# Optimization experiments

Measured on AMD Instinct MI355X. Metric: run time of the kernel, lower is better.

Reference implementation:

```python
import jax, jax.numpy as jnp
import numpy as np

B, N, DEG = 64, 256, 16          # graphs, nodes per graph, avg degree
FIN, OUT, DEP, HID = 256, 256, 64, 256
E = B * N * DEG                   # 262144 edges (no self loops)
NN = B * N                        # 16384 total nodes


def setup_inputs() -> dict:
    key = jax.random.key(0)
    ks = jax.random.split(key, 12)
    s = 0.05
    x = jax.random.normal(ks[0], (NN, FIN), jnp.float32)
    # random edges within each graph block, guaranteed no self loops
    src = jax.random.randint(ks[1], (E,), 0, N)
    dst = (src + jax.random.randint(ks[2], (E,), 1, N)) % N
    gid = jnp.repeat(jnp.arange(B) * N, N * DEG)
    edge_index = jnp.stack([src + gid, dst + gid]).astype(jnp.int32)
    edge_attr = jax.random.normal(ks[3], (E, DEP), jnp.float32)
    WA = jax.random.normal(ks[4], (OUT, FIN), jnp.float32) * s
    WB = jax.random.normal(ks[5], (OUT, DEP), jnp.float32) * s
    gcn_bias = jnp.zeros((OUT,), jnp.float32)

    def gru_p(k, insz):
        k1, k2, k3, k4 = jax.random.split(k, 4)
        return (jax.random.normal(k1, (3 * HID, insz), jnp.float32) * s,
                jax.random.normal(k2, (3 * HID, HID), jnp.float32) * s,
                jax.random.normal(k3, (3 * HID,), jnp.float32) * s,
                jax.random.normal(k4, (3 * HID,), jnp.float32) * s)

    w_ih0, w_hh0, b_ih0, b_hh0 = gru_p(ks[6], OUT)
    w_ih1, w_hh1, b_ih1, b_hh1 = gru_p(ks[7], HID)
    w_ih2, w_hh2, b_ih2, b_hh2 = gru_p(ks[8], HID)
    lin_W = jax.random.normal(ks[9], (2, 5 * HID), jnp.float32) * s
    lin_b = jnp.zeros((2,), jnp.float32)
    return dict(x=x, edge_attr=edge_attr, edge_index=edge_index, WA=WA, WB=WB,
                gcn_bias=gcn_bias,
                w_ih0=w_ih0, w_hh0=w_hh0, b_ih0=b_ih0, b_hh0=b_hh0,
                w_ih1=w_ih1, w_hh1=w_hh1, b_ih1=b_ih1, b_hh1=b_hh1,
                w_ih2=w_ih2, w_hh2=w_hh2, b_ih2=b_ih2, b_hh2=b_hh2,
                lin_W=lin_W, lin_b=lin_b)


def _gru_layer(seq, w_ih, w_hh, b_ih, b_hh):
    # seq: [B, T, in] -> ([B, T, HID], final h [B, HID]); torch GRU gate math
    xp = jnp.einsum('bti,gi->btg', seq, w_ih) + b_ih  # precompute input projections

    def step(h, xt):
        gh = h @ w_hh.T + b_hh
        xr, xz, xn = jnp.split(xt, 3, axis=-1)
        hr, hz, hn = jnp.split(gh, 3, axis=-1)
        r = jax.nn.sigmoid(xr + hr)
        z = jax.nn.sigmoid(xz + hz)
        n = jnp.tanh(xn + r * hn)
        h = (1.0 - z) * n + z * h
        return h, h

    h0 = jnp.zeros((seq.shape[0], HID), seq.dtype)
    hT, ys = jax.lax.scan(step, h0, jnp.swapaxes(xp, 0, 1))
    return jnp.swapaxes(ys, 0, 1), hT


def _forward(x, edge_attr, WA, WB, gcn_bias,
             w_ih0, w_hh0, b_ih0, b_hh0,
             w_ih1, w_hh1, b_ih1, b_hh1,
             w_ih2, w_hh2, b_ih2, b_hh2,
             lin_W, lin_b, edge_index):
    # --- myGCNConv: add_remaining_self_loops (none exist), degree norm ---
    loop = jnp.arange(NN, dtype=edge_index.dtype)
    row = jnp.concatenate([edge_index[0], loop])
    col = jnp.concatenate([edge_index[1], loop])
    ea = jnp.concatenate([edge_attr, jnp.ones((NN, DEP), edge_attr.dtype)], axis=0)
    deg = jax.ops.segment_sum(jnp.ones(row.shape, x.dtype), col, num_segments=NN)
    dinv = jnp.where(deg > 0, deg ** -0.5, 0.0)
    norm = dinv[row] * dinv[col]
    # message: norm * tanh(A(x_j) * B(edge_attr)); project nodes once, gather
    Ax = (x @ WA.T)[row]                       # [E+NN, OUT]
    Be = ea @ WB.T                             # [E+NN, OUT]
    msg = norm[:, None] * jnp.tanh(Ax * Be)
    # aggr='mean': scatter-sum / incoming-degree (>=1 after self loops)
    agg = jax.ops.segment_sum(msg, col, num_segments=NN) / jnp.maximum(deg, 1.0)[:, None]
    node = jnp.tanh(agg + gcn_bias)            # model-level Tanh

    # --- GRU (3 layers) over per-graph node sequences (equal lengths) ---
    seq = node.reshape(B, N, OUT)
    hts = []
    for p in ((w_ih0, w_hh0, b_ih0, b_hh0),
              (w_ih1, w_hh1, b_ih1, b_hh1),
              (w_ih2, w_hh2, b_ih2, b_hh2)):
        seq, hT = _gru_layer(seq, *p)
        hts.append(hT)

    avg_pool = seq.sum(axis=1) / N
    max_pool = seq.max(axis=1)
    pool = jnp.concatenate(hts + [max_pool, avg_pool], axis=1)  # [B, 5*HID]
    return jax.nn.softmax(pool @ lin_W.T + lin_b, axis=1)


def reference(x, edge_attr, edge_index, WA, WB, gcn_bias,
              w_ih0, w_hh0, b_ih0, b_hh0,
              w_ih1, w_hh1, b_ih1, b_hh1,
              w_ih2, w_hh2, b_ih2, b_hh2,
              lin_W, lin_b):
    return _forward(x, edge_attr, WA, WB, gcn_bias,
                    w_ih0, w_hh0, b_ih0, b_hh0,
                    w_ih1, w_hh1, b_ih1, b_hh1,
                    w_ih2, w_hh2, b_ih2, b_hh2,
                    lin_W, lin_b, edge_index)
```

## Files before the change

kernel.cpp:

```cpp
#include <hip/hip_runtime.h>
#include <math.h>

#define NN   16384
#define NE   262144
#define NB   64
#define SEQT 256
#define DEP  64
#define DOUT 256
#define G3   768
#define GK   256
#define ECAP 32

typedef _Float16 h2_t   __attribute__((ext_vector_type(2)));
typedef _Float16 f16x4  __attribute__((ext_vector_type(4)));
typedef _Float16 f16x8  __attribute__((ext_vector_type(8)));
typedef float    f32x4  __attribute__((ext_vector_type(4)));

static __device__ __forceinline__ h2_t pk(float a, float b) {
    return (h2_t)__builtin_amdgcn_cvt_pkrtz(a, b);
}

static __device__ __forceinline__ float fast_sigmoid(float v) {
    return __builtin_amdgcn_rcpf(1.f + __expf(-v));
}
static __device__ __forceinline__ float fast_tanh(float v) {
    return 1.f - 2.f * __builtin_amdgcn_rcpf(1.f + __expf(2.f * v));
}

static __device__ __forceinline__ void bar_lds() {
    asm volatile("s_waitcnt lgkmcnt(0)\n\ts_barrier" ::: "memory");
}

__global__ void k_count(const int* __restrict__ ei, int* deg) {
    int e = blockIdx.x * 256 + threadIdx.x;
    if (e < NE) atomicAdd(&deg[ei[NE + e]], 1);
}

__global__ __launch_bounds__(1024) void k_scan_offs(const int* __restrict__ deg,
                                                    int* __restrict__ offs,
                                                    float* __restrict__ dinv) {
    __shared__ int lds[1024];
    const int tid = threadIdx.x;
    const int v0 = tid * 16;
    int loc[16];
    int s = 0;
#pragma unroll
    for (int i = 0; i < 16; ++i) {
        int d = deg[v0 + i];
        loc[i] = s;
        s += d;
        dinv[v0 + i] = rsqrtf((float)(d + 1));
    }
    lds[tid] = s;
    __syncthreads();
    for (int off = 1; off < 1024; off <<= 1) {
        int x = (tid >= off) ? lds[tid - off] : 0;
        __syncthreads();
        lds[tid] += x;
        __syncthreads();
    }
    int base = lds[tid] - s;
#pragma unroll
    for (int i = 0; i < 16; ++i) offs[v0 + i] = base + loc[i];
}

__global__ void k_fill(const int* __restrict__ ei, const int* __restrict__ offs,
                       int* cursor, int* __restrict__ eidx) {
    int e = blockIdx.x * 256 + threadIdx.x;
    if (e < NE) {
        int c = ei[NE + e];
        int pos = offs[c] + atomicAdd(&cursor[c], 1);
        eidx[pos] = e;
    }
}

__global__ void k_bself(const float* __restrict__ WB, float* Bself) {
    int f = threadIdx.x;
    float s = 0.f;
#pragma unroll
    for (int d = 0; d < DEP; ++d) s += WB[f * DEP + d];
    Bself[f] = s;
}

__global__ void k_bias_fold(const float* __restrict__ bi0, const float* __restrict__ bh0,
                            const float* __restrict__ bi1, const float* __restrict__ bh1,
                            const float* __restrict__ bi2, const float* __restrict__ bh2,
                            float* __restrict__ o) {
    int j = blockIdx.x * 256 + threadIdx.x;
    int l = j / G3, r = j % G3;
    const float* bi = (l == 0) ? bi0 : (l == 1) ? bi1 : bi2;
    const float* bh = (l == 0) ? bh0 : (l == 1) ? bh1 : bh2;
    o[j] = bi[r] + (r < 512 ? bh[r] : 0.f);
}

__global__ void k_cvt_all(const float* __restrict__ x,  const float* __restrict__ wa,
                          const float* __restrict__ w0, const float* __restrict__ w1,
                          const float* __restrict__ w2,
                          _Float16* __restrict__ xo,  _Float16* __restrict__ wao,
                          _Float16* __restrict__ w0o, _Float16* __restrict__ w1o,
                          _Float16* __restrict__ w2o) {
    size_t i = ((size_t)blockIdx.x * 256 + threadIdx.x) * 4;
    const size_t B0 = 4194304, B1 = B0 + 65536, B2 = B1 + 196608, B3 = B2 + 196608;
    const float* in; _Float16* out; size_t off;
    if      (i < B0) { in = x;  out = xo;  off = i; }
    else if (i < B1) { in = wa; out = wao; off = i - B0; }
    else if (i < B2) { in = w0; out = w0o; off = i - B1; }
    else if (i < B3) { in = w1; out = w1o; off = i - B2; }
    else             { in = w2; out = w2o; off = i - B3; }
    float4 v = *(const float4*)(in + off);
    *(h2_t*)(out + off)     = pk(v.x, v.y);
    *(h2_t*)(out + off + 2) = pk(v.z, v.w);
}

template <bool F16OUT>
__global__ __launch_bounds__(256) void k_gemm16(const _Float16* __restrict__ A16,
                                                const _Float16* __restrict__ B16,
                                                const float* __restrict__ bias,
                                                void* __restrict__ Cout,
                                                int M, int N) {
    const int tid  = threadIdx.x;
    const int lane = tid & 63;
    const int wv   = tid >> 6;
    const int m0   = blockIdx.x * 128 + wv * 32;
    const int n0   = blockIdx.y * 128;
    const int ml   = lane & 15;
    const int quad = lane >> 4;

    const _Float16* ap0 = A16 + (size_t)(m0 + ml) * GK + quad * 8;
    const _Float16* ap1 = ap0 + (size_t)16 * GK;
    const _Float16* bp0 = B16 + (size_t)(n0 + ml) * GK + quad * 8;

    f32x4 acc[2][8];
#pragma unroll
    for (int i = 0; i < 2; ++i)
#pragma unroll
        for (int j = 0; j < 8; ++j) acc[i][j] = (f32x4){0.f, 0.f, 0.f, 0.f};

#pragma unroll 2
    for (int k0 = 0; k0 < GK; k0 += 32) {
        f16x8 a0 = *(const f16x8*)(ap0 + k0);
        f16x8 a1 = *(const f16x8*)(ap1 + k0);
#pragma unroll
        for (int nf = 0; nf < 8; ++nf) {
            f16x8 bf = *(const f16x8*)(bp0 + (size_t)nf * 16 * GK + k0);
            acc[0][nf] = __builtin_amdgcn_mfma_f32_16x16x32_f16(a0, bf, acc[0][nf], 0, 0, 0);
            acc[1][nf] = __builtin_amdgcn_mfma_f32_16x16x32_f16(a1, bf, acc[1][nf], 0, 0, 0);
        }
    }

#pragma unroll
    for (int mf = 0; mf < 2; ++mf)
#pragma unroll
        for (int nf = 0; nf < 8; ++nf) {
            const int col = n0 + nf * 16 + ml;
            const float bv = bias ? bias[col] : 0.f;
#pragma unroll
            for (int r = 0; r < 4; ++r) {
                const int row = m0 + mf * 16 + quad * 4 + r;
                float v = acc[mf][nf][r] + bv;
                if (F16OUT)
                    ((_Float16*)Cout)[(size_t)row * N + col] = (_Float16)v;
                else
                    ((float*)Cout)[(size_t)row * N + col] = v;
            }
        }
}

__global__ __launch_bounds__(256) void k_gcn(const float* __restrict__ Ax,
                                             const float* __restrict__ WB,
                                             const float* __restrict__ edge_attr,
                                             const int* __restrict__ ei,
                                             const int* __restrict__ eidx,
                                             const int* __restrict__ offs,
                                             const int* __restrict__ deg,
                                             const float* __restrict__ dinv,
                                             const float* __restrict__ Bself,
                                             const float* __restrict__ gcn_bias,
                                             _Float16* __restrict__ node16) {
    const int v = blockIdx.x;
    const int f = threadIdx.x;

    float wb[64];
#pragma unroll
    for (int d4 = 0; d4 < 16; ++d4) {
        float4 t = *(const float4*)&WB[f * DEP + d4 * 4];
        wb[d4 * 4 + 0] = t.x; wb[d4 * 4 + 1] = t.y;
        wb[d4 * 4 + 2] = t.z; wb[d4 * 4 + 3] = t.w;
    }

    __shared__ float ea_s[ECAP * 64];
    __shared__ int   es_s[ECAP];
    __shared__ int   src_s[ECAP];
    __shared__ float nrm_s[ECAP];

    const int   base = offs[v];
    const int   cnt  = deg[v];
    const float dv   = dinv[v];
    float acc = 0.f;

    for (int c0 = 0; c0 < cnt; c0 += ECAP) {
        const int n = min(ECAP, cnt - c0);
        if (f < n) {
            int e = eidx[base + c0 + f];
            es_s[f] = e;
            int s = ei[e];
            src_s[f] = s;
            nrm_s[f] = dinv[s] * dv;
        }
        __syncthreads();
        for (int idx = f; idx < n * 64; idx += 256) {
            int el = idx >> 6, d = idx & 63;
            ea_s[idx] = edge_attr[(size_t)es_s[el] * DEP + d];
        }
        __syncthreads();
        for (int i = 0; i < n; ++i) {
            float ax = Ax[(size_t)src_s[i] * DOUT + f];
            float be = 0.f;
#pragma unroll
            for (int d = 0; d < 64; ++d) be = fmaf(wb[d], ea_s[i * 64 + d], be);
            acc = fmaf(nrm_s[i], fast_tanh(ax * be), acc);
        }
        __syncthreads();
    }
    acc += dv * dv * fast_tanh(Ax[(size_t)v * DOUT + f] * Bself[f]);
    float nv = fast_tanh(acc / (float)(cnt + 1) + gcn_bias[f]);
    node16[(size_t)v * DOUT + f] = (_Float16)nv;
}

__global__ __launch_bounds__(512, 2) void k_gru_scan(const _Float16* __restrict__ xp16,
                                                     const float* __restrict__ w_hh,
                                                     const float* __restrict__ b_hh,
                                                     _Float16* __restrict__ y16,
                                                     float* __restrict__ hT_all,
                                                     int layer,
                                                     const float* __restrict__ lin_W,
                                                     const float* __restrict__ lin_b,
                                                     float* __restrict__ out) {
    const int tid  = threadIdx.x;
    const int b    = blockIdx.x;
    const int lane = tid & 63;
    const int wv   = tid >> 6;
    const int m    = lane & 15;
    const int quad = lane >> 4;
    const int p    = (m >> 3) & 1;
    const int rsel = m & 3;
    const int j    = wv * 32 + p * 16 + quad * 4 + rsel;
    const bool wr  = (m & 4) == 0;

    f16x8 A[6][8];
#pragma unroll
    for (int rb = 0; rb < 6; ++rb) {
        const int lr  = rb * 16 + m;
        const int row = ((lr >> 5) << 8) + wv * 32 + (lr & 31);
#pragma unroll
        for (int kt = 0; kt < 8; ++kt) {
            const float* wp = w_hh + (size_t)row * 256 + kt * 32 + quad * 8;
            float4 a0 = *(const float4*)wp;
            float4 a1 = *(const float4*)(wp + 4);
            union { f16x8 v; h2_t h[4]; } u;
            u.h[0] = pk(a0.x, a0.y); u.h[1] = pk(a0.z, a0.w);
            u.h[2] = pk(a1.x, a1.y); u.h[3] = pk(a1.z, a1.w);
            A[rb][kt] = u.v;
        }
    }

    const float bhn = b_hh[512 + j];

    __shared__ _Float16 h16[2][256];
    __shared__ float    pool[1280];
    __shared__ float    red[512];

    float h_old = 0.f;
    if (tid < 256) h16[0][tid] = (_Float16)0.f;
    __syncthreads();

    const _Float16* xpb  = xp16 + (size_t)b * SEQT * G3;
    _Float16*       yb16 = y16  + (size_t)b * SEQT * DOUT;

    float mx = -1e30f, sm = 0.f;

    _Float16 pxr = xpb[j], pxz = xpb[256 + j], pxn = xpb[512 + j];

    for (int t = 0; t < SEQT; ++t) {
        const float xr = (float)pxr;
        const float xz = (float)pxz;
        const float xn = (float)pxn;
        {
            const _Float16* xq = xpb + (size_t)(t + 1) * G3 + j;
            pxr = xq[0]; pxz = xq[256]; pxn = xq[512];
        }

        const _Float16* hcur = h16[t & 1];
        f32x4 C[6];
#pragma unroll
        for (int rb = 0; rb < 6; ++rb) C[rb] = (f32x4){0.f, 0.f, 0.f, 0.f};

#pragma unroll
        for (int kt = 0; kt < 8; ++kt) {
            union { f16x8 v; float4 f; } Bk;
            Bk.f = *(const float4*)&hcur[kt * 32 + quad * 8];
#pragma unroll
            for (int rb = 0; rb < 6; ++rb)
                C[rb] = __builtin_amdgcn_mfma_f32_16x16x32_f16(A[rb][kt], Bk.v, C[rb], 0, 0, 0);
        }

        float gh[3];
#pragma unroll
        for (int g = 0; g < 3; ++g) {
            const float lo01 = (rsel & 1) ? C[2 * g][1] : C[2 * g][0];
            const float lo23 = (rsel & 1) ? C[2 * g][3] : C[2 * g][2];
            const float lo   = (rsel & 2) ? lo23 : lo01;
            const float hi01 = (rsel & 1) ? C[2 * g + 1][1] : C[2 * g + 1][0];
            const float hi23 = (rsel & 1) ? C[2 * g + 1][3] : C[2 * g + 1][2];
            const float hi   = (rsel & 2) ? hi23 : hi01;
            gh[g] = p ? hi : lo;
        }

        const float r  = fast_sigmoid(xr + gh[0]);
        const float z  = fast_sigmoid(xz + gh[1]);
        const float n  = fast_tanh(xn + r * (gh[2] + bhn));
        const float hn = n + z * (h_old - n);
        h_old = hn;
        if (wr) {
            h16[(t & 1) ^ 1][j] = (_Float16)hn;
            if (layer < 2) {
                yb16[(size_t)t * DOUT + j] = (_Float16)hn;
                if (t == SEQT - 1) hT_all[layer * NB * 256 + b * 256 + j] = hn;
            }
        }
        if (layer == 2) { mx = fmaxf(mx, hn); sm += hn; }

        bar_lds();
    }

    if (layer == 2) {
        if (wr) {
            pool[j]        = hT_all[b * 256 + j];
            pool[256 + j]  = hT_all[NB * 256 + b * 256 + j];
            pool[512 + j]  = h_old;
            pool[768 + j]  = mx;
            pool[1024 + j] = sm * (1.f / 256.f);
        }
        __syncthreads();
        if (tid < 256) {
            float p0 = 0.f, p1 = 0.f;
            for (int i = tid; i < 1280; i += 256) {
                float pv = pool[i];
                p0 = fmaf(lin_W[i], pv, p0);
                p1 = fmaf(lin_W[1280 + i], pv, p1);
            }
            red[tid] = p0; red[256 + tid] = p1;
        }
        __syncthreads();
        if (tid == 0) {
            float l0 = lin_b[0], l1 = lin_b[1];
            for (int i = 0; i < 256; ++i) { l0 += red[i]; l1 += red[256 + i]; }
            float m2 = fmaxf(l0, l1);
            float e0 = __expf(l0 - m2), e1 = __expf(l1 - m2);
            float s = e0 + e1;
            out[b * 2 + 0] = e0 / s;
            out[b * 2 + 1] = e1 / s;
        }
    }
}

extern "C" void kernel_launch(void* const* d_in, const int* in_sizes, int n_in,
                              void* d_out, int out_size, void* d_ws, size_t ws_size,
                              hipStream_t stream) {
    const float* x         = (const float*)d_in[0];
    const float* edge_attr = (const float*)d_in[1];
    const int*   ei        = (const int*)d_in[2];
    const float* WA        = (const float*)d_in[3];
    const float* WB        = (const float*)d_in[4];
    const float* gcn_bias  = (const float*)d_in[5];
    const float* w_ih[3] = {(const float*)d_in[6],  (const float*)d_in[10], (const float*)d_in[14]};
    const float* w_hh[3] = {(const float*)d_in[7],  (const float*)d_in[11], (const float*)d_in[15]};
    const float* b_ih[3] = {(const float*)d_in[8],  (const float*)d_in[12], (const float*)d_in[16]};
    const float* b_hh[3] = {(const float*)d_in[9],  (const float*)d_in[13], (const float*)d_in[17]};
    const float* lin_W = (const float*)d_in[18];
    const float* lin_b = (const float*)d_in[19];
    float* out = (float*)d_out;

    char* p = (char*)d_ws;
    auto alloc = [&](size_t bytes) {
        char* r = p;
        p += (bytes + 255) & ~(size_t)255;
        return r;
    };
    int*   deg    = (int*)alloc((size_t)NN * 4);
    int*   offs   = (int*)alloc((size_t)NN * 4);
    int*   cursor = (int*)alloc((size_t)NN * 4);
    float* dinv   = (float*)alloc((size_t)NN * 4);
    int*   eidx   = (int*)alloc((size_t)NE * 4);
    float* Bself  = (float*)alloc(256 * 4);
    float* hT     = (float*)alloc(2 * NB * 256 * 4);
    float* bias768 = (float*)alloc(3 * G3 * 4);
    float* Ax     = (float*)alloc((size_t)NN * DOUT * 4);
    _Float16* xp16 = (_Float16*)alloc((size_t)NN * G3 * 2);

    _Float16* node16 = (_Float16*)alloc((size_t)NN * DOUT * 2);
    _Float16* yA16   = (_Float16*)alloc((size_t)NN * DOUT * 2);
    _Float16* x16    = (_Float16*)alloc((size_t)NN * DOUT * 2);
    _Float16* yB16   = x16;
    _Float16* WA16   = (_Float16*)alloc((size_t)256 * 256 * 2);
    _Float16* wih16[3];
    for (int l = 0; l < 3; ++l) wih16[l] = (_Float16*)alloc((size_t)G3 * 256 * 2);

    hipMemsetAsync(deg, 0, (size_t)3 * NN * 4, stream);
    k_count<<<NE / 256, 256, 0, stream>>>(ei, deg);
    k_scan_offs<<<1, 1024, 0, stream>>>(deg, offs, dinv);
    k_fill<<<NE / 256, 256, 0, stream>>>(ei, offs, cursor, eidx);
    k_bself<<<1, 256, 0, stream>>>(WB, Bself);
    k_bias_fold<<<9, 256, 0, stream>>>(b_ih[0], b_hh[0], b_ih[1], b_hh[1],
                                       b_ih[2], b_hh[2], bias768);
    k_cvt_all<<<4736, 256, 0, stream>>>(x, WA, w_ih[0], w_ih[1], w_ih[2],
                                        x16, WA16, wih16[0], wih16[1], wih16[2]);

    {
        dim3 g(NN / 128, 256 / 128);
        k_gemm16<false><<<g, 256, 0, stream>>>(x16, WA16, nullptr, Ax, NN, 256);
    }
    k_gcn<<<NN, 256, 0, stream>>>(Ax, WB, edge_attr, ei, eidx, offs, deg, dinv,
                                  Bself, gcn_bias, node16);

    const _Float16* in16 = node16;
    _Float16* y16_outs[3] = {yA16, yB16, yA16};
    for (int l = 0; l < 3; ++l) {
        dim3 g(NN / 128, G3 / 128);
        k_gemm16<true><<<g, 256, 0, stream>>>(in16, wih16[l], bias768 + l * G3,
                                              xp16, NN, G3);
        k_gru_scan<<<NB, 512, 0, stream>>>(xp16, w_hh[l], b_hh[l], y16_outs[l],
                                           hT, l, lin_W, lin_b, out);
        in16 = y16_outs[l];
    }
}
```

Measured before the change: 1.405 ms.

## Precompute edge-attribute projection with MFMA GEMM instead of per-edge dot products in GCN

Converts edge_attr and WB to fp16 and runs a dedicated MFMA GEMM producing a per-edge 256-wide projection Be16, so the GCN kernel reads one value per edge-feature instead of doing a 64-term FMA dot product per thread per edge. The GEMM kernel is templated on K, and the edge chunk size ECAP is raised. The cost is an extra 128 MB fp16 buffer that is written and then read back, plus a larger conversion pass over edge_attr and reduced precision on the edge term.

Result: faster. 1.261 ms (-10.3%).

```diff
diff --git a/kernel.cpp b/kernel.cpp
--- a/kernel.cpp
+++ b/kernel.cpp
@@ -8,8 +8,7 @@
 #define DEP  64
 #define DOUT 256
 #define G3   768
-#define GK   256
-#define ECAP 32
+#define ECAP 64
 
 typedef _Float16 h2_t   __attribute__((ext_vector_type(2)));
 typedef _Float16 f16x4  __attribute__((ext_vector_type(4)));
@@ -95,24 +94,33 @@
 
 __global__ void k_cvt_all(const float* __restrict__ x,  const float* __restrict__ wa,
                           const float* __restrict__ w0, const float* __restrict__ w1,
-                          const float* __restrict__ w2,
+                          const float* __restrict__ w2, const float* __restrict__ ea,
+                          const float* __restrict__ wb,
                           _Float16* __restrict__ xo,  _Float16* __restrict__ wao,
                           _Float16* __restrict__ w0o, _Float16* __restrict__ w1o,
-                          _Float16* __restrict__ w2o) {
+                          _Float16* __restrict__ w2o, _Float16* __restrict__ eao,
+                          _Float16* __restrict__ wbo) {
     size_t i = ((size_t)blockIdx.x * 256 + threadIdx.x) * 4;
-    const size_t B0 = 4194304, B1 = B0 + 65536, B2 = B1 + 196608, B3 = B2 + 196608;
+    const size_t B0 = 4194304;
+    const size_t B1 = B0 + 65536;
+    const size_t B2 = B1 + 196608;
+    const size_t B3 = B2 + 196608;
+    const size_t B4 = B3 + 196608;
+    const size_t B5 = B4 + 16777216;
     const float* in; _Float16* out; size_t off;
     if      (i < B0) { in = x;  out = xo;  off = i; }
     else if (i < B1) { in = wa; out = wao; off = i - B0; }
     else if (i < B2) { in = w0; out = w0o; off = i - B1; }
     else if (i < B3) { in = w1; out = w1o; off = i - B2; }
-    else             { in = w2; out = w2o; off = i - B3; }
+    else if (i < B4) { in = w2; out = w2o; off = i - B3; }
+    else if (i < B5) { in = ea; out = eao; off = i - B4; }
+    else             { in = wb; out = wbo; off = i - B5; }
     float4 v = *(const float4*)(in + off);
     *(h2_t*)(out + off)     = pk(v.x, v.y);
     *(h2_t*)(out + off + 2) = pk(v.z, v.w);
 }
 
-template <bool F16OUT>
+template <int K, bool F16OUT>
 __global__ __launch_bounds__(256) void k_gemm16(const _Float16* __restrict__ A16,
                                                 const _Float16* __restrict__ B16,
                                                 const float* __restrict__ bias,
@@ -126,9 +134,9 @@
     const int ml   = lane & 15;
     const int quad = lane >> 4;
 
-    const _Float16* ap0 = A16 + (size_t)(m0 + ml) * GK + quad * 8;
-    const _Float16* ap1 = ap0 + (size_t)16 * GK;
-    const _Float16* bp0 = B16 + (size_t)(n0 + ml) * GK + quad * 8;
+    const _Float16* ap0 = A16 + (size_t)(m0 + ml) * K + quad * 8;
+    const _Float16* ap1 = ap0 + (size_t)16 * K;
+    const _Float16* bp0 = B16 + (size_t)(n0 + ml) * K + quad * 8;
 
     f32x4 acc[2][8];
 #pragma unroll
@@ -137,12 +145,12 @@
         for (int j = 0; j < 8; ++j) acc[i][j] = (f32x4){0.f, 0.f, 0.f, 0.f};
 
 #pragma unroll 2
-    for (int k0 = 0; k0 < GK; k0 += 32) {
+    for (int k0 = 0; k0 < K; k0 += 32) {
         f16x8 a0 = *(const f16x8*)(ap0 + k0);
         f16x8 a1 = *(const f16x8*)(ap1 + k0);
 #pragma unroll
         for (int nf = 0; nf < 8; ++nf) {
-            f16x8 bf = *(const f16x8*)(bp0 + (size_t)nf * 16 * GK + k0);
+            f16x8 bf = *(const f16x8*)(bp0 + (size_t)nf * 16 * K + k0);
             acc[0][nf] = __builtin_amdgcn_mfma_f32_16x16x32_f16(a0, bf, acc[0][nf], 0, 0, 0);
             acc[1][nf] = __builtin_amdgcn_mfma_f32_16x16x32_f16(a1, bf, acc[1][nf], 0, 0, 0);
         }
@@ -167,8 +175,7 @@
 }
 
 __global__ __launch_bounds__(256) void k_gcn(const float* __restrict__ Ax,
-                                             const float* __restrict__ WB,
-                                             const float* __restrict__ edge_attr,
+                                             const _Float16* __restrict__ Be16,
                                              const int* __restrict__ ei,
                                              const int* __restrict__ eidx,
                                              const int* __restrict__ offs,
@@ -180,15 +187,6 @@
     const int v = blockIdx.x;
     const int f = threadIdx.x;
 
-    float wb[64];
-#pragma unroll
-    for (int d4 = 0; d4 < 16; ++d4) {
-        float4 t = *(const float4*)&WB[f * DEP + d4 * 4];
-        wb[d4 * 4 + 0] = t.x; wb[d4 * 4 + 1] = t.y;
-        wb[d4 * 4 + 2] = t.z; wb[d4 * 4 + 3] = t.w;
-    }
-
-    __shared__ float ea_s[ECAP * 64];
     __shared__ int   es_s[ECAP];
     __shared__ int   src_s[ECAP];
     __shared__ float nrm_s[ECAP];
@@ -208,16 +206,10 @@
             nrm_s[f] = dinv[s] * dv;
         }
         __syncthreads();
-        for (int idx = f; idx < n * 64; idx += 256) {
-            int el = idx >> 6, d = idx & 63;
-            ea_s[idx] = edge_attr[(size_t)es_s[el] * DEP + d];
-        }
-        __syncthreads();
+#pragma unroll 4
         for (int i = 0; i < n; ++i) {
             float ax = Ax[(size_t)src_s[i] * DOUT + f];
-            float be = 0.f;
-#pragma unroll
-            for (int d = 0; d < 64; ++d) be = fmaf(wb[d], ea_s[i * 64 + d], be);
+            float be = (float)Be16[(size_t)es_s[i] * DOUT + f];
             acc = fmaf(nrm_s[i], fast_tanh(ax * be), acc);
         }
         __syncthreads();
@@ -405,6 +397,9 @@
     _Float16* WA16   = (_Float16*)alloc((size_t)256 * 256 * 2);
     _Float16* wih16[3];
     for (int l = 0; l < 3; ++l) wih16[l] = (_Float16*)alloc((size_t)G3 * 256 * 2);
+    _Float16* ea16 = (_Float16*)alloc((size_t)NE * DEP * 2);
+    _Float16* WB16 = (_Float16*)alloc((size_t)256 * DEP * 2);
+    _Float16* Be16 = (_Float16*)alloc((size_t)NE * DOUT * 2);
 
     hipMemsetAsync(deg, 0, (size_t)3 * NN * 4, stream);
     k_count<<<NE / 256, 256, 0, stream>>>(ei, deg);
@@ -413,22 +408,28 @@
     k_bself<<<1, 256, 0, stream>>>(WB, Bself);
     k_bias_fold<<<9, 256, 0, stream>>>(b_ih[0], b_hh[0], b_ih[1], b_hh[1],
                                        b_ih[2], b_hh[2], bias768);
-    k_cvt_all<<<4736, 256, 0, stream>>>(x, WA, w_ih[0], w_ih[1], w_ih[2],
-                                        x16, WA16, wih16[0], wih16[1], wih16[2]);
+    k_cvt_all<<<21136, 256, 0, stream>>>(x, WA, w_ih[0], w_ih[1], w_ih[2],
+                                         edge_attr, WB,
+                                         x16, WA16, wih16[0], wih16[1], wih16[2],
+                                         ea16, WB16);
 
     {
         dim3 g(NN / 128, 256 / 128);
-        k_gemm16<false><<<g, 256, 0, stream>>>(x16, WA16, nullptr, Ax, NN, 256);
-    }
-    k_gcn<<<NN, 256, 0, stream>>>(Ax, WB, edge_attr, ei, eidx, offs, deg, dinv,
+        k_gemm16<256, false><<<g, 256, 0, stream>>>(x16, WA16, nullptr, Ax, NN, 256);
+    }
+    {
+        dim3 g(NE / 128, 256 / 128);
+        k_gemm16<64, true><<<g, 256, 0, stream>>>(ea16, WB16, nullptr, Be16, NE, 256);
+    }
+    k_gcn<<<NN, 256, 0, stream>>>(Ax, Be16, ei, eidx, offs, deg, dinv,
                                   Bself, gcn_bias, node16);
 
     const _Float16* in16 = node16;
     _Float16* y16_outs[3] = {yA16, yB16, yA16};
     for (int l = 0; l < 3; ++l) {
         dim3 g(NN / 128, G3 / 128);
-        k_gemm16<true><<<g, 256, 0, stream>>>(in16, wih16[l], bias768 + l * G3,
-                                              xp16, NN, G3);
+        k_gemm16<256, true><<<g, 256, 0, stream>>>(in16, wih16[l], bias768 + l * G3,
+                                                   xp16, NN, G3);
         k_gru_scan<<<NB, 512, 0, stream>>>(xp16, w_hh[l], b_hh[l], y16_outs[l],
                                            hT, l, lin_W, lin_b, out);
         in16 = y16_outs[l];
```
